# Performance work log

Hardware: AMD Instinct MI355X
Metric: run time of the kernel (lower is better)

## Reference

```python
import jax, jax.numpy as jnp
import numpy as np

N, B, H, OUT, T = 200000, 1024, 256, 128, 2  # nodes, graphs, hidden(=in_dim), out_dim, timesteps
NEG_SLOPE = 0.01


def setup_inputs() -> dict:
    key = jax.random.key(0)
    ks = jax.random.split(key, 12)
    s = 0.05
    f32 = jnp.float32
    return {
        "x": jax.random.normal(ks[0], (N, H), dtype=f32),
        "batch": jnp.sort(jax.random.randint(ks[1], (N,), 0, B)),
        # GATConv params (heads=1, shared lin for src/dst since in_channels is int)
        "W": jax.random.normal(ks[2], (H, H), dtype=f32) * s,
        "att_src": jax.random.normal(ks[3], (H,), dtype=f32) * s,
        "att_dst": jax.random.normal(ks[4], (H,), dtype=f32) * s,
        "bias_gat": jnp.zeros((H,), dtype=f32),
        # GRUCell params (input_size = H, hidden_size = H)
        "W_ih": jax.random.normal(ks[5], (3 * H, H), dtype=f32) * s,
        "W_hh": jax.random.normal(ks[6], (3 * H, H), dtype=f32) * s,
        "b_ih": jnp.zeros((3 * H,), dtype=f32),
        "b_hh": jnp.zeros((3 * H,), dtype=f32),
        # final Linear
        "W_lin": jax.random.normal(ks[7], (H, OUT), dtype=f32) * s,
        "b_lin": jnp.zeros((OUT,), dtype=f32),
    }


def reference(x, batch, W, att_src, att_dst, bias_gat, W_ih, W_hh, b_ih, b_hh, W_lin, b_lin):
    # out = global_add_pool(x, batch)  -> [B, H]
    out = jax.ops.segment_sum(x, batch, num_segments=B)
    for _ in range(T):
        # --- bipartite GATConv((x, out), edge_index=[arange(N), batch]) ---
        xs = x @ W                       # [N, H] transformed source nodes
        od = out @ W                     # [B, H] transformed dst (graph) nodes
        a_src = xs @ att_src             # [N]
        a_dst = od @ att_dst             # [B]
        e = a_src + a_dst[batch]         # [N] per-edge raw score (one edge per node)
        e = jnp.where(e > 0, e, NEG_SLOPE * e)  # leaky_relu(negative_slope=0.01)
        # scatter-softmax over each graph's incoming edges
        emax = jax.ops.segment_max(e, batch, num_segments=B)
        ee = jnp.exp(e - emax[batch])
        denom = jax.ops.segment_sum(ee, batch, num_segments=B)
        alpha = ee / denom[batch]        # [N]
        # scatter-add aggregation of weighted messages
        agg = jax.ops.segment_sum(xs * alpha[:, None], batch, num_segments=B) + bias_gat
        h = jax.nn.elu(agg)              # [B, H]  (dropout is identity in eval)
        # --- GRUCell(h, out) ---
        gi = h @ W_ih.T + b_ih           # [B, 3H]
        gh = out @ W_hh.T + b_hh         # [B, 3H]
        r = jax.nn.sigmoid(gi[:, :H] + gh[:, :H])
        z = jax.nn.sigmoid(gi[:, H:2 * H] + gh[:, H:2 * H])
        n = jnp.tanh(gi[:, 2 * H:] + r * gh[:, 2 * H:])
        out = jax.nn.silu((1.0 - z) * n + z * out)  # activation = F.silu
    return out @ W_lin + b_lin           # [B, OUT]
```

## Files before the change

### kernel.cpp

```cpp
#include <hip/hip_runtime.h>
#include <math.h>

#define N_NODES 200000
#define BGRAPH  1024
#define HDIM    256
#define ODIM    128
#define TSTEPS  2

#define ACT_NONE 0
#define ACT_ELU  1

__global__ void k_vectors(const float* __restrict__ W, const float* __restrict__ att_src,
                          const float* __restrict__ att_dst, float* __restrict__ v,
                          float* __restrict__ u) {
    int i = threadIdx.x;
    float sv = 0.f, su = 0.f;
    for (int j = 0; j < HDIM; ++j) {
        float w = W[i * HDIM + j];
        sv += w * att_src[j];
        su += w * att_dst[j];
    }
    v[i] = sv; u[i] = su;
}

__global__ void k_bounds(const int* __restrict__ batch, int* __restrict__ seg) {
    int b = blockIdx.x * blockDim.x + threadIdx.x;
    if (b > BGRAPH) return;
    if (b == BGRAPH) { seg[b] = N_NODES; return; }
    int lo = 0, hi = N_NODES;
    while (lo < hi) { int mid = (lo + hi) >> 1; if (batch[mid] < b) lo = mid + 1; else hi = mid; }
    seg[b] = lo;
}

__global__ __launch_bounds__(256) void k_passA(const float* __restrict__ x,
        const int* __restrict__ seg, const float* __restrict__ v,
        float* __restrict__ s, float* __restrict__ stt) {
    int b = blockIdx.x;
    int lo = seg[b], hi = seg[b + 1];
    int t = threadIdx.x, wave = t >> 6, lane = t & 63;
    float v0 = v[4 * lane + 0], v1 = v[4 * lane + 1], v2 = v[4 * lane + 2], v3 = v[4 * lane + 3];
    float p0 = 0.f, p1 = 0.f, p2 = 0.f, p3 = 0.f;
    for (int i = lo + wave; i < hi; i += 4) {
        const float4 r = *(const float4*)(x + (size_t)i * HDIM + 4 * lane);
        p0 += r.x; p1 += r.y; p2 += r.z; p3 += r.w;
        float part = r.x * v0 + r.y * v1 + r.z * v2 + r.w * v3;
        #pragma unroll
        for (int off = 32; off > 0; off >>= 1) part += __shfl_down(part, off, 64);
        if (lane == 0) s[i] = part;
    }
    __shared__ float comb[4][HDIM];
    comb[wave][4 * lane + 0] = p0; comb[wave][4 * lane + 1] = p1;
    comb[wave][4 * lane + 2] = p2; comb[wave][4 * lane + 3] = p3;
    __syncthreads();
    stt[(size_t)b * HDIM + t] = comb[0][t] + comb[1][t] + comb[2][t] + comb[3][t];
}

__global__ __launch_bounds__(256) void k_iter(const float* __restrict__ x,
        const int* __restrict__ seg, const float* __restrict__ s,
        const float* __restrict__ u, const float* __restrict__ stt,
        float* __restrict__ aggx) {
    int b = blockIdx.x, t = threadIdx.x;
    int lo = seg[b], hi = seg[b + 1];
    __shared__ float red[256];
    red[t] = stt[(size_t)b * HDIM + t] * u[t];
    __syncthreads();
    for (int st = 128; st > 0; st >>= 1) { if (t < st) red[t] += red[t + st]; __syncthreads(); }
    float d = red[0];
    __syncthreads();
    float m = -3.402823466e38f;
    for (int i = lo + t; i < hi; i += 256) {
        float e = s[i] + d; e = e > 0.f ? e : 0.01f * e;
        m = fmaxf(m, e);
    }
    red[t] = m; __syncthreads();
    for (int st = 128; st > 0; st >>= 1) { if (t < st) red[t] = fmaxf(red[t], red[t + st]); __syncthreads(); }
    float M = red[0];
    __syncthreads();
    float sm = 0.f;
    for (int i = lo + t; i < hi; i += 256) {
        float e = s[i] + d; e = e > 0.f ? e : 0.01f * e;
        sm += __expf(e - M);
    }
    red[t] = sm; __syncthreads();
    for (int st = 128; st > 0; st >>= 1) { if (t < st) red[t] += red[t + st]; __syncthreads(); }
    float inv = (hi > lo) ? 1.0f / red[0] : 0.f;
    __syncthreads();
    int wave = t >> 6, lane = t & 63;
    float a0 = 0.f, a1 = 0.f, a2 = 0.f, a3 = 0.f;
    for (int i = lo + wave; i < hi; i += 4) {
        float e = s[i] + d; e = e > 0.f ? e : 0.01f * e;
        float alpha = __expf(e - M) * inv;
        const float4 r = *(const float4*)(x + (size_t)i * HDIM + 4 * lane);
        a0 += alpha * r.x; a1 += alpha * r.y; a2 += alpha * r.z; a3 += alpha * r.w;
    }
    __shared__ float comb[4][HDIM];
    comb[wave][4 * lane + 0] = a0; comb[wave][4 * lane + 1] = a1;
    comb[wave][4 * lane + 2] = a2; comb[wave][4 * lane + 3] = a3;
    __syncthreads();
    aggx[(size_t)b * HDIM + t] = comb[0][t] + comb[1][t] + comb[2][t] + comb[3][t];
}

template<bool BT, int ACT>
__global__ __launch_bounds__(256) void k_gemm(const float* __restrict__ A,
        const float* __restrict__ B, const float* __restrict__ bias,
        float* __restrict__ C, int M, int N, int K) {
    __shared__ __align__(16) float As[16][64];
    __shared__ __align__(16) float Bs[16][64];
    int tx = threadIdx.x & 15, ty = threadIdx.x >> 4;
    int m0 = blockIdx.x * 64, n0 = blockIdx.y * 64;
    float acc[4][4] = {};
    for (int k0 = 0; k0 < K; k0 += 16) {
        {
            int r = threadIdx.x >> 2;
            int kk = (threadIdx.x & 3) << 2;
            float4 av = *(const float4*)(A + (size_t)(m0 + r) * K + k0 + kk);
            As[kk + 0][r] = av.x; As[kk + 1][r] = av.y;
            As[kk + 2][r] = av.z; As[kk + 3][r] = av.w;
        }
        if (BT) {
            int r = threadIdx.x >> 2;
            int kk = (threadIdx.x & 3) << 2;
            float4 bv = *(const float4*)(B + (size_t)(n0 + r) * K + k0 + kk);
            Bs[kk + 0][r] = bv.x; Bs[kk + 1][r] = bv.y;
            Bs[kk + 2][r] = bv.z; Bs[kk + 3][r] = bv.w;
        } else {
            int kk = threadIdx.x >> 4;
            int nn = (threadIdx.x & 15) << 2;
            float4 bv = *(const float4*)(B + (size_t)(k0 + kk) * N + n0 + nn);
            Bs[kk][nn + 0] = bv.x; Bs[kk][nn + 1] = bv.y;
            Bs[kk][nn + 2] = bv.z; Bs[kk][nn + 3] = bv.w;
        }
        __syncthreads();
        #pragma unroll
        for (int kk = 0; kk < 16; ++kk) {
            float4 a = *(const float4*)&As[kk][ty * 4];
            float4 bb = *(const float4*)&Bs[kk][tx * 4];
            acc[0][0] += a.x * bb.x; acc[0][1] += a.x * bb.y; acc[0][2] += a.x * bb.z; acc[0][3] += a.x * bb.w;
            acc[1][0] += a.y * bb.x; acc[1][1] += a.y * bb.y; acc[1][2] += a.y * bb.z; acc[1][3] += a.y * bb.w;
            acc[2][0] += a.z * bb.x; acc[2][1] += a.z * bb.y; acc[2][2] += a.z * bb.z; acc[2][3] += a.z * bb.w;
            acc[3][0] += a.w * bb.x; acc[3][1] += a.w * bb.y; acc[3][2] += a.w * bb.z; acc[3][3] += a.w * bb.w;
        }
        __syncthreads();
    }
    float bsv[4];
    #pragma unroll
    for (int j = 0; j < 4; ++j) bsv[j] = bias[n0 + tx * 4 + j];
    #pragma unroll
    for (int i = 0; i < 4; ++i) {
        int m = m0 + ty * 4 + i;
        float vout[4];
        #pragma unroll
        for (int j = 0; j < 4; ++j) {
            float vv = acc[i][j] + bsv[j];
            if (ACT == ACT_ELU) vv = vv > 0.f ? vv : expm1f(vv);
            vout[j] = vv;
        }
        *(float4*)(C + (size_t)m * N + n0 + tx * 4) =
            make_float4(vout[0], vout[1], vout[2], vout[3]);
    }
}

__global__ __launch_bounds__(256) void k_gru(const float* __restrict__ gi,
        const float* __restrict__ gh, float* __restrict__ stt) {
    int idx = blockIdx.x * 256 + threadIdx.x;
    int b = idx >> 8, j = idx & 255;
    size_t base = (size_t)b * (3 * HDIM);
    float gir = gi[base + j], giz = gi[base + HDIM + j], gin = gi[base + 2 * HDIM + j];
    float ghr = gh[base + j], ghz = gh[base + HDIM + j], ghn = gh[base + 2 * HDIM + j];
    float r = 1.f / (1.f + __expf(-(gir + ghr)));
    float z = 1.f / (1.f + __expf(-(giz + ghz)));
    float n = tanhf(gin + r * ghn);
    float prev = stt[idx];
    float h2 = (1.f - z) * n + z * prev;
    stt[idx] = h2 / (1.f + __expf(-h2));
}

extern "C" void kernel_launch(void* const* d_in, const int* in_sizes, int n_in,
                              void* d_out, int out_size, void* d_ws, size_t ws_size,
                              hipStream_t stream) {
    const float* x        = (const float*)d_in[0];
    const int*   batch    = (const int*)d_in[1];
    const float* W        = (const float*)d_in[2];
    const float* att_src  = (const float*)d_in[3];
    const float* att_dst  = (const float*)d_in[4];
    const float* bias_gat = (const float*)d_in[5];
    const float* W_ih     = (const float*)d_in[6];
    const float* W_hh     = (const float*)d_in[7];
    const float* b_ih     = (const float*)d_in[8];
    const float* b_hh     = (const float*)d_in[9];
    const float* W_lin    = (const float*)d_in[10];
    const float* b_lin    = (const float*)d_in[11];

    char* ws = (char*)d_ws;
    size_t off = 0;
    auto alloc = [&](size_t bytes) {
        void* p = (void*)(ws + off);
        off += (bytes + 255) & ~(size_t)255;
        return p;
    };
    float* s    = (float*)alloc((size_t)N_NODES * 4);
    int*   seg  = (int*)alloc((BGRAPH + 1) * 4);
    float* vv   = (float*)alloc(HDIM * 4);
    float* uu   = (float*)alloc(HDIM * 4);
    float* stt  = (float*)alloc((size_t)BGRAPH * HDIM * 4);
    float* aggx = (float*)alloc((size_t)BGRAPH * HDIM * 4);
    float* hbuf = (float*)alloc((size_t)BGRAPH * HDIM * 4);
    float* gi   = (float*)alloc((size_t)BGRAPH * 3 * HDIM * 4);
    float* gh   = (float*)alloc((size_t)BGRAPH * 3 * HDIM * 4);

    hipLaunchKernelGGL(k_vectors, dim3(1), dim3(HDIM), 0, stream, W, att_src, att_dst, vv, uu);
    hipLaunchKernelGGL(k_bounds, dim3(5), dim3(256), 0, stream, batch, seg);
    hipLaunchKernelGGL(k_passA, dim3(BGRAPH), dim3(256), 0, stream, x, seg, vv, s, stt);

    for (int tstep = 0; tstep < TSTEPS; ++tstep) {
        hipLaunchKernelGGL(k_iter, dim3(BGRAPH), dim3(256), 0, stream, x, seg, s, uu, stt, aggx);
        hipLaunchKernelGGL((k_gemm<false, ACT_ELU>), dim3(BGRAPH / 64, HDIM / 64), dim3(256), 0,
                           stream, aggx, W, bias_gat, hbuf, BGRAPH, HDIM, HDIM);
        hipLaunchKernelGGL((k_gemm<true, ACT_NONE>), dim3(BGRAPH / 64, (3 * HDIM) / 64), dim3(256), 0,
                           stream, hbuf, W_ih, b_ih, gi, BGRAPH, 3 * HDIM, HDIM);
        hipLaunchKernelGGL((k_gemm<true, ACT_NONE>), dim3(BGRAPH / 64, (3 * HDIM) / 64), dim3(256), 0,
                           stream, stt, W_hh, b_hh, gh, BGRAPH, 3 * HDIM, HDIM);
        hipLaunchKernelGGL(k_gru, dim3(BGRAPH * HDIM / 256), dim3(256), 0, stream, gi, gh, stt);
    }
    hipLaunchKernelGGL((k_gemm<false, ACT_NONE>), dim3(BGRAPH / 64, ODIM / 64), dim3(256), 0,
                       stream, stt, W_lin, b_lin, (float*)d_out, BGRAPH, ODIM, HDIM);
}
```

Before: 522.3 us.

## Fuse GAT linear+ELU into aggregation kernel, batch GRU GEMMs, unroll node loops

The per-graph attention aggregation kernel now also does the 256x256 W matvec, bias and ELU for its graph, so the separate tiled GEMM launch and the aggx round trip go away. The two GRU GEMMs (input and hidden) run as one launch using a z-dimension of 2, with biases moved into the GRU elementwise kernel. The node loops in the pooling and aggregation kernels are unrolled by two rows to keep more loads in flight. The fused matvec reads W once per block from global or cache without tiling, which may cost more than the shared-memory tiled GEMM it replaces.

```diff
diff --git a/kernel.cpp b/kernel.cpp
--- a/kernel.cpp
+++ b/kernel.cpp
@@ -40,13 +40,27 @@
     int t = threadIdx.x, wave = t >> 6, lane = t & 63;
     float v0 = v[4 * lane + 0], v1 = v[4 * lane + 1], v2 = v[4 * lane + 2], v3 = v[4 * lane + 3];
     float p0 = 0.f, p1 = 0.f, p2 = 0.f, p3 = 0.f;
-    for (int i = lo + wave; i < hi; i += 4) {
-        const float4 r = *(const float4*)(x + (size_t)i * HDIM + 4 * lane);
-        p0 += r.x; p1 += r.y; p2 += r.z; p3 += r.w;
-        float part = r.x * v0 + r.y * v1 + r.z * v2 + r.w * v3;
-        #pragma unroll
-        for (int off = 32; off > 0; off >>= 1) part += __shfl_down(part, off, 64);
-        if (lane == 0) s[i] = part;
+    int i = lo + wave;
+    for (; i + 4 < hi; i += 8) {
+        const float4 r0 = *(const float4*)(x + (size_t)i * HDIM + 4 * lane);
+        const float4 r1 = *(const float4*)(x + (size_t)(i + 4) * HDIM + 4 * lane);
+        p0 += r0.x + r1.x; p1 += r0.y + r1.y; p2 += r0.z + r1.z; p3 += r0.w + r1.w;
+        float pa = r0.x * v0 + r0.y * v1 + r0.z * v2 + r0.w * v3;
+        float pb = r1.x * v0 + r1.y * v1 + r1.z * v2 + r1.w * v3;
+        #pragma unroll
+        for (int off = 32; off > 0; off >>= 1) {
+            pa += __shfl_down(pa, off, 64);
+            pb += __shfl_down(pb, off, 64);
+        }
+        if (lane == 0) { s[i] = pa; s[i + 4] = pb; }
+    }
+    for (; i < hi; i += 4) {
+        const float4 r0 = *(const float4*)(x + (size_t)i * HDIM + 4 * lane);
+        p0 += r0.x; p1 += r0.y; p2 += r0.z; p3 += r0.w;
+        float pa = r0.x * v0 + r0.y * v1 + r0.z * v2 + r0.w * v3;
+        #pragma unroll
+        for (int off = 32; off > 0; off >>= 1) pa += __shfl_down(pa, off, 64);
+        if (lane == 0) s[i] = pa;
     }
     __shared__ float comb[4][HDIM];
     comb[wave][4 * lane + 0] = p0; comb[wave][4 * lane + 1] = p1;
@@ -55,10 +69,11 @@
     stt[(size_t)b * HDIM + t] = comb[0][t] + comb[1][t] + comb[2][t] + comb[3][t];
 }
 
-__global__ __launch_bounds__(256) void k_iter(const float* __restrict__ x,
+__global__ __launch_bounds__(256) void k_iter_h(const float* __restrict__ x,
         const int* __restrict__ seg, const float* __restrict__ s,
         const float* __restrict__ u, const float* __restrict__ stt,
-        float* __restrict__ aggx) {
+        const float* __restrict__ W, const float* __restrict__ bias_gat,
+        float* __restrict__ hbuf) {
     int b = blockIdx.x, t = threadIdx.x;
     int lo = seg[b], hi = seg[b + 1];
     __shared__ float red[256];
@@ -87,21 +102,80 @@
     __syncthreads();
     int wave = t >> 6, lane = t & 63;
     float a0 = 0.f, a1 = 0.f, a2 = 0.f, a3 = 0.f;
-    for (int i = lo + wave; i < hi; i += 4) {
-        float e = s[i] + d; e = e > 0.f ? e : 0.01f * e;
-        float alpha = __expf(e - M) * inv;
-        const float4 r = *(const float4*)(x + (size_t)i * HDIM + 4 * lane);
-        a0 += alpha * r.x; a1 += alpha * r.y; a2 += alpha * r.z; a3 += alpha * r.w;
+    int i = lo + wave;
+    for (; i + 4 < hi; i += 8) {
+        float e0 = s[i] + d;     e0 = e0 > 0.f ? e0 : 0.01f * e0;
+        float e1 = s[i + 4] + d; e1 = e1 > 0.f ? e1 : 0.01f * e1;
+        float al0 = __expf(e0 - M) * inv;
+        float al1 = __expf(e1 - M) * inv;
+        const float4 r0 = *(const float4*)(x + (size_t)i * HDIM + 4 * lane);
+        const float4 r1 = *(const float4*)(x + (size_t)(i + 4) * HDIM + 4 * lane);
+        a0 += al0 * r0.x + al1 * r1.x; a1 += al0 * r0.y + al1 * r1.y;
+        a2 += al0 * r0.z + al1 * r1.z; a3 += al0 * r0.w + al1 * r1.w;
+    }
+    for (; i < hi; i += 4) {
+        float e0 = s[i] + d; e0 = e0 > 0.f ? e0 : 0.01f * e0;
+        float al0 = __expf(e0 - M) * inv;
+        const float4 r0 = *(const float4*)(x + (size_t)i * HDIM + 4 * lane);
+        a0 += al0 * r0.x; a1 += al0 * r0.y; a2 += al0 * r0.z; a3 += al0 * r0.w;
     }
     __shared__ float comb[4][HDIM];
     comb[wave][4 * lane + 0] = a0; comb[wave][4 * lane + 1] = a1;
     comb[wave][4 * lane + 2] = a2; comb[wave][4 * lane + 3] = a3;
     __syncthreads();
-    aggx[(size_t)b * HDIM + t] = comb[0][t] + comb[1][t] + comb[2][t] + comb[3][t];
-}
-
-template<bool BT, int ACT>
-__global__ __launch_bounds__(256) void k_gemm(const float* __restrict__ A,
+    __shared__ float ax[HDIM];
+    ax[t] = comb[0][t] + comb[1][t] + comb[2][t] + comb[3][t];
+    __syncthreads();
+    float acc = bias_gat[t];
+    #pragma unroll 8
+    for (int ii = 0; ii < HDIM; ++ii) acc += ax[ii] * W[(size_t)ii * HDIM + t];
+    hbuf[(size_t)b * HDIM + t] = acc > 0.f ? acc : expm1f(acc);
+}
+
+__global__ __launch_bounds__(256) void k_gemm2(const float* __restrict__ A0,
+        const float* __restrict__ A1, const float* __restrict__ B0,
+        const float* __restrict__ B1, float* __restrict__ C0, float* __restrict__ C1,
+        int M, int N, int K) {
+    const float* A = blockIdx.z ? A1 : A0;
+    const float* B = blockIdx.z ? B1 : B0;
+    float* C = blockIdx.z ? C1 : C0;
+    __shared__ __align__(16) float As[16][64];
+    __shared__ __align__(16) float Bs[16][64];
+    int tx = threadIdx.x & 15, ty = threadIdx.x >> 4;
+    int m0 = blockIdx.x * 64, n0 = blockIdx.y * 64;
+    float acc[4][4] = {};
+    for (int k0 = 0; k0 < K; k0 += 16) {
+        {
+            int r = threadIdx.x >> 2;
+            int kk = (threadIdx.x & 3) << 2;
+            float4 av = *(const float4*)(A + (size_t)(m0 + r) * K + k0 + kk);
+            As[kk + 0][r] = av.x; As[kk + 1][r] = av.y;
+            As[kk + 2][r] = av.z; As[kk + 3][r] = av.w;
+            float4 bv = *(const float4*)(B + (size_t)(n0 + r) * K + k0 + kk);
+            Bs[kk + 0][r] = bv.x; Bs[kk + 1][r] = bv.y;
+            Bs[kk + 2][r] = bv.z; Bs[kk + 3][r] = bv.w;
+        }
+        __syncthreads();
+        #pragma unroll
+        for (int kk = 0; kk < 16; ++kk) {
+            float4 a = *(const float4*)&As[kk][ty * 4];
+            float4 bb = *(const float4*)&Bs[kk][tx * 4];
+            acc[0][0] += a.x * bb.x; acc[0][1] += a.x * bb.y; acc[0][2] += a.x * bb.z; acc[0][3] += a.x * bb.w;
+            acc[1][0] += a.y * bb.x; acc[1][1] += a.y * bb.y; acc[1][2] += a.y * bb.z; acc[1][3] += a.y * bb.w;
+            acc[2][0] += a.z * bb.x; acc[2][1] += a.z * bb.y; acc[2][2] += a.z * bb.z; acc[2][3] += a.z * bb.w;
+            acc[3][0] += a.w * bb.x; acc[3][1] += a.w * bb.y; acc[3][2] += a.w * bb.z; acc[3][3] += a.w * bb.w;
+        }
+        __syncthreads();
+    }
+    #pragma unroll
+    for (int i = 0; i < 4; ++i) {
+        int mrow = m0 + ty * 4 + i;
+        *(float4*)(C + (size_t)mrow * N + n0 + tx * 4) =
+            make_float4(acc[i][0], acc[i][1], acc[i][2], acc[i][3]);
+    }
+}
+
+__global__ __launch_bounds__(256) void k_gemm_nn(const float* __restrict__ A,
         const float* __restrict__ B, const float* __restrict__ bias,
         float* __restrict__ C, int M, int N, int K) {
     __shared__ __align__(16) float As[16][64];
@@ -117,13 +191,7 @@
             As[kk + 0][r] = av.x; As[kk + 1][r] = av.y;
             As[kk + 2][r] = av.z; As[kk + 3][r] = av.w;
         }
-        if (BT) {
-            int r = threadIdx.x >> 2;
-            int kk = (threadIdx.x & 3) << 2;
-            float4 bv = *(const float4*)(B + (size_t)(n0 + r) * K + k0 + kk);
-            Bs[kk + 0][r] = bv.x; Bs[kk + 1][r] = bv.y;
-            Bs[kk + 2][r] = bv.z; Bs[kk + 3][r] = bv.w;
-        } else {
+        {
             int kk = threadIdx.x >> 4;
             int nn = (threadIdx.x & 15) << 2;
             float4 bv = *(const float4*)(B + (size_t)(k0 + kk) * N + n0 + nn);
@@ -147,26 +215,25 @@
     for (int j = 0; j < 4; ++j) bsv[j] = bias[n0 + tx * 4 + j];
     #pragma unroll
     for (int i = 0; i < 4; ++i) {
-        int m = m0 + ty * 4 + i;
-        float vout[4];
-        #pragma unroll
-        for (int j = 0; j < 4; ++j) {
-            float vv = acc[i][j] + bsv[j];
-            if (ACT == ACT_ELU) vv = vv > 0.f ? vv : expm1f(vv);
-            vout[j] = vv;
-        }
-        *(float4*)(C + (size_t)m * N + n0 + tx * 4) =
-            make_float4(vout[0], vout[1], vout[2], vout[3]);
+        int mrow = m0 + ty * 4 + i;
+        *(float4*)(C + (size_t)mrow * N + n0 + tx * 4) =
+            make_float4(acc[i][0] + bsv[0], acc[i][1] + bsv[1],
+                        acc[i][2] + bsv[2], acc[i][3] + bsv[3]);
     }
 }
 
 __global__ __launch_bounds__(256) void k_gru(const float* __restrict__ gi,
-        const float* __restrict__ gh, float* __restrict__ stt) {
+        const float* __restrict__ gh, const float* __restrict__ b_ih,
+        const float* __restrict__ b_hh, float* __restrict__ stt) {
     int idx = blockIdx.x * 256 + threadIdx.x;
-    int b = idx >> 8, j = idx & 255;
-    size_t base = (size_t)b * (3 * HDIM);
-    float gir = gi[base + j], giz = gi[base + HDIM + j], gin = gi[base + 2 * HDIM + j];
-    float ghr = gh[base + j], ghz = gh[base + HDIM + j], ghn = gh[base + 2 * HDIM + j];
+    int j = idx & 255;
+    size_t base = (size_t)(idx >> 8) * (3 * HDIM);
+    float gir = gi[base + j] + b_ih[j];
+    float giz = gi[base + HDIM + j] + b_ih[HDIM + j];
+    float gin = gi[base + 2 * HDIM + j] + b_ih[2 * HDIM + j];
+    float ghr = gh[base + j] + b_hh[j];
+    float ghz = gh[base + HDIM + j] + b_hh[HDIM + j];
+    float ghn = gh[base + 2 * HDIM + j] + b_hh[2 * HDIM + j];
     float r = 1.f / (1.f + __expf(-(gir + ghr)));
     float z = 1.f / (1.f + __expf(-(giz + ghz)));
     float n = tanhf(gin + r * ghn);
@@ -203,7 +270,6 @@
     float* vv   = (float*)alloc(HDIM * 4);
     float* uu   = (float*)alloc(HDIM * 4);
     float* stt  = (float*)alloc((size_t)BGRAPH * HDIM * 4);
-    float* aggx = (float*)alloc((size_t)BGRAPH * HDIM * 4);
     float* hbuf = (float*)alloc((size_t)BGRAPH * HDIM * 4);
     float* gi   = (float*)alloc((size_t)BGRAPH * 3 * HDIM * 4);
     float* gh   = (float*)alloc((size_t)BGRAPH * 3 * HDIM * 4);
@@ -213,15 +279,13 @@
     hipLaunchKernelGGL(k_passA, dim3(BGRAPH), dim3(256), 0, stream, x, seg, vv, s, stt);
 
     for (int tstep = 0; tstep < TSTEPS; ++tstep) {
-        hipLaunchKernelGGL(k_iter, dim3(BGRAPH), dim3(256), 0, stream, x, seg, s, uu, stt, aggx);
-        hipLaunchKernelGGL((k_gemm<false, ACT_ELU>), dim3(BGRAPH / 64, HDIM / 64), dim3(256), 0,
-                           stream, aggx, W, bias_gat, hbuf, BGRAPH, HDIM, HDIM);
-        hipLaunchKernelGGL((k_gemm<true, ACT_NONE>), dim3(BGRAPH / 64, (3 * HDIM) / 64), dim3(256), 0,
-                           stream, hbuf, W_ih, b_ih, gi, BGRAPH, 3 * HDIM, HDIM);
-        hipLaunchKernelGGL((k_gemm<true, ACT_NONE>), dim3(BGRAPH / 64, (3 * HDIM) / 64), dim3(256), 0,
-                           stream, stt, W_hh, b_hh, gh, BGRAPH, 3 * HDIM, HDIM);
-        hipLaunchKernelGGL(k_gru, dim3(BGRAPH * HDIM / 256), dim3(256), 0, stream, gi, gh, stt);
-    }
-    hipLaunchKernelGGL((k_gemm<false, ACT_NONE>), dim3(BGRAPH / 64, ODIM / 64), dim3(256), 0,
+        hipLaunchKernelGGL(k_iter_h, dim3(BGRAPH), dim3(256), 0, stream,
+                           x, seg, s, uu, stt, W, bias_gat, hbuf);
+        hipLaunchKernelGGL(k_gemm2, dim3(BGRAPH / 64, (3 * HDIM) / 64, 2), dim3(256), 0,
+                           stream, hbuf, stt, W_ih, W_hh, gi, gh, BGRAPH, 3 * HDIM, HDIM);
+        hipLaunchKernelGGL(k_gru, dim3(BGRAPH * HDIM / 256), dim3(256), 0, stream,
+                           gi, gh, b_ih, b_hh, stt);
+    }
+    hipLaunchKernelGGL(k_gemm_nn, dim3(BGRAPH / 64, ODIM / 64), dim3(256), 0,
                        stream, stt, W_lin, b_lin, (float*)d_out, BGRAPH, ODIM, HDIM);
 }
```

Measured after the change: 484.2 us. 1.08x faster.
